# Performance work log

Measured on AMD Instinct MI355X. Metric: run time of the kernel, lower is better.

Reference implementation:

```python
import jax, jax.numpy as jnp
import numpy as np
from jax import lax

B = 32
ITERS = 100
ALPHA = 0.3  # keras LeakyReLU default alpha
BN_SCALE = np.float32(1.0 / np.sqrt(1.0 + 1e-3))  # inference BN, default moving stats (mean 0, var 1)


def _make_psf_mat():
    # Gaussian PSF mapping 5184 fine (72x72) code positions -> 81 coarse (9x9) pixels, mat shape (5184, 81)
    sigma = (150.0 / 100.0) * 9.0 / 64.0
    coarse = np.arange(9) + 0.5
    fine = (np.arange(72) + 0.5) * 9.0 / 72.0
    g = np.exp(-(fine[:, None] - coarse[None, :]) ** 2 / (2.0 * sigma ** 2))  # (72, 9)
    mat = np.einsum('ia,jb->ijab', g, g).reshape(5184, 81)
    mat = mat / np.linalg.norm(mat, ord=2)  # spectral-normalize so FISTA (mu=1) is stable
    return mat.astype(np.float32)


def leaky(x):
    return jnp.where(x >= 0, x, ALPHA * x)


def conv(x, k, strides=(1, 1)):
    return lax.conv_general_dilated(x, k, strides, 'SAME',
                                    dimension_numbers=('NHWC', 'HWIO', 'NHWC'))


def _forward(inp, mat, w1_k, w1_b, x1_k, x1_b, c51_k, c51_b, c15_k, c15_b,
             c55_k, c55_b, x2_k, x2_b, y17_k, y17_b, y71_k, y71_b, yc_k, yc_b,
             d1_k, d2_k, h1_w, h1_b, h2_w, h2_b, h3_w, h3_b):
    b = inp.shape[0]
    # w branch
    w = leaky(conv(inp, w1_k) + w1_b)  # (B,9,9,1)
    # z branch -> lambda parameter
    z = inp * BN_SCALE
    z = leaky(conv(z, d1_k, strides=(3, 3)) * BN_SCALE)  # (B,3,3,12), downsample: conv no-bias + BN + LeakyReLU
    z = leaky(conv(z, d2_k, strides=(3, 3)) * BN_SCALE)  # (B,1,1,24)
    z = z.reshape(b, -1)
    z = z @ h1_w + h1_b
    z = z @ h2_w + h2_b
    z = z @ h3_w + h3_b  # (B,1)
    param = 0.1 * jax.nn.sigmoid(z)  # (B,1)
    # x branch: normalize (max of |x| over axis 1 only, as in source)
    x = inp / (0.001 + jnp.max(jnp.abs(inp), axis=1, keepdims=True))
    x = leaky(conv(x, x1_k) + x1_b)  # (B,9,9,3)
    # --- CompressedSensing: 100-iter FISTA, vectorized over batch and 3 channels ---
    im = x.reshape(b, 81, 3).transpose(0, 2, 1)  # (B,3,81) row-major flatten per channel
    lam = (param * 0.1)[:, :, None]  # (B,1,1), mu = 1.0

    def step(carry, _):
        y_tmp, y_last, t = carry
        resid = im - jnp.einsum('bcn,nk->bck', y_tmp, mat)      # (B,3,81)  = im - mat^T y
        re = jnp.einsum('bck,nk->bcn', resid, mat)              # (B,3,5184) = mat (im - mat^T y)
        wv = y_tmp + re
        y_new = jax.nn.relu(wv - lam) - jax.nn.relu(-wv - lam)  # soft threshold
        t_n = (1.0 + jnp.sqrt(1.0 + 4.0 * t * t)) / 2.0
        y_next = y_new + (t - 1.0) / t_n * (y_new - y_last)
        return (y_next, y_new, t_n), None

    init = (jnp.zeros((b, 3, 5184), jnp.float32),
            jnp.zeros((b, 3, 5184), jnp.float32),
            jnp.float32(1.0))
    (_, y_new, _), _ = lax.scan(step, init, None, length=ITERS)
    cs_out = y_new.transpose(0, 2, 1).reshape(b, 72, 72, 3)  # stack channels last then reshape
    x = conv(cs_out, c51_k, strides=(2, 2)) + c51_b   # (B,36,36,16), no activation
    x = conv(x, c15_k, strides=(2, 2)) + c15_b        # (B,18,18,32)
    x = conv(x, c55_k, strides=(2, 2)) + c55_b        # (B,9,9,64)
    x = leaky(conv(x, x2_k) + x2_b)                   # (B,9,9,8)
    # y branch
    y1 = conv(inp, y17_k) + y17_b                     # (B,9,9,32)
    y2 = conv(inp, y71_k) + y71_b                     # (B,9,9,32)
    y = leaky(conv(jnp.concatenate([y1, y2], axis=-1), yc_k) + yc_b)  # (B,9,9,32)
    out = jnp.concatenate([w, x, y], axis=-1)         # (B,9,9,41)
    return out, cs_out


def setup_inputs() -> dict:
    key = jax.random.key(0)
    ks = jax.random.split(key, 20)
    rn = lambda k, s, sc=0.1: sc * jax.random.normal(k, s, dtype=jnp.float32)
    x1_k = jnp.clip(1.0 + 0.3 * jax.random.normal(ks[1], (1, 1, 3, 3)), 0.0, None).astype(jnp.float32)
    return {
        'inp': jax.random.normal(ks[0], (B, 9, 9, 3), dtype=jnp.float32),
        'mat': jnp.asarray(_make_psf_mat()),
        'w1_k': rn(ks[2], (1, 1, 3, 1)), 'w1_b': jnp.zeros((1,), jnp.float32),
        'x1_k': x1_k, 'x1_b': jnp.zeros((3,), jnp.float32),
        'c51_k': rn(ks[3], (5, 1, 3, 16)), 'c51_b': jnp.zeros((16,), jnp.float32),
        'c15_k': rn(ks[4], (1, 5, 16, 32)), 'c15_b': jnp.zeros((32,), jnp.float32),
        'c55_k': rn(ks[5], (5, 5, 32, 64)), 'c55_b': jnp.zeros((64,), jnp.float32),
        'x2_k': rn(ks[6], (1, 1, 64, 8)), 'x2_b': jnp.zeros((8,), jnp.float32),
        'y17_k': rn(ks[7], (1, 7, 3, 32)), 'y17_b': jnp.zeros((32,), jnp.float32),
        'y71_k': rn(ks[8], (7, 1, 3, 32)), 'y71_b': jnp.zeros((32,), jnp.float32),
        'yc_k': rn(ks[9], (1, 1, 64, 32)), 'yc_b': jnp.zeros((32,), jnp.float32),
        'd1_k': rn(ks[10], (5, 5, 3, 12)), 'd2_k': rn(ks[11], (5, 5, 12, 24)),
        'h1_w': rn(ks[12], (24, 24), 0.2), 'h1_b': jnp.zeros((24,), jnp.float32),
        'h2_w': rn(ks[13], (24, 12), 0.2), 'h2_b': jnp.zeros((12,), jnp.float32),
        'h3_w': rn(ks[14], (12, 1), 0.2), 'h3_b': jnp.zeros((1,), jnp.float32),
    }


def reference(inp, mat, w1_k, w1_b, x1_k, x1_b, c51_k, c51_b, c15_k, c15_b,
              c55_k, c55_b, x2_k, x2_b, y17_k, y17_b, y71_k, y71_b, yc_k, yc_b,
              d1_k, d2_k, h1_w, h1_b, h2_w, h2_b, h3_w, h3_b):
    return _forward(inp, mat, w1_k, w1_b, x1_k, x1_b, c51_k, c51_b, c15_k, c15_b,
                    c55_k, c55_b, x2_k, x2_b, y17_k, y17_b, y71_k, y71_b, yc_k, yc_b,
                    d1_k, d2_k, h1_w, h1_b, h2_w, h2_b, h3_w, h3_b)
```

## Files before the change

kernel.cpp:

```cpp
#include <hip/hip_runtime.h>
#include <math.h>

#define LEAKY(x) ((x) >= 0.f ? (x) : 0.3f*(x))

#define G_OFF   0
#define IM_OFF  648
#define LAM_OFF 8424
#define WB_OFF  8456
#define YBR_OFF 11048
#define X1_OFF  93992
#define X2_OFF  757544
#define X3_OFF  1089320

#define OUT0 106272

__global__ __launch_bounds__(256) void prep_kernel(
    const float* __restrict__ inp, const float* __restrict__ mat,
    const float* __restrict__ w1_k, const float* __restrict__ w1_b,
    const float* __restrict__ x1_k, const float* __restrict__ x1_b,
    const float* __restrict__ y17_k, const float* __restrict__ y17_b,
    const float* __restrict__ y71_k, const float* __restrict__ y71_b,
    const float* __restrict__ yc_k, const float* __restrict__ yc_b,
    const float* __restrict__ d1_k, const float* __restrict__ d2_k,
    const float* __restrict__ h1_w, const float* __restrict__ h1_b,
    const float* __restrict__ h2_w, const float* __restrict__ h2_b,
    const float* __restrict__ h3_w, const float* __restrict__ h3_b,
    float* __restrict__ ws)
{
    int t = threadIdx.x;
    if (blockIdx.x == 0) {
        float rs = rsqrtf(mat[0]);
        for (int u = t; u < 648; u += 256) {
            int i = u / 9, a = u % 9;
            ws[G_OFF + u] = mat[(size_t)(i*72)*81 + a*9] * rs;
        }
        return;
    }
    int b = blockIdx.x - 1;
    __shared__ float sin_[243];
    __shared__ float cm[27];
    __shared__ float cat[5184];
    __shared__ float z1[108];
    __shared__ float z2[24];
    __shared__ float v1[24];
    __shared__ float v2[12];

    const float BN  = 1.0f / sqrtf(1.001f);
    const float BN2 = BN * BN;

    for (int u = t; u < 243; u += 256) sin_[u] = inp[b*243 + u];
    __syncthreads();

    if (t < 81) {
        float s = w1_b[0];
        for (int i = 0; i < 3; ++i) s += sin_[t*3+i] * w1_k[i];
        ws[WB_OFF + b*81 + t] = LEAKY(s);
    } else if (t < 108) {
        int u = t - 81;
        float m = 0.f;
        for (int r = 0; r < 9; ++r) m = fmaxf(m, fabsf(sin_[r*27 + u]));
        cm[u] = 0.001f + m;
    }
    if (t >= 128 && t < 236) {
        int u = t - 128;
        int o = u % 12, ox = (u/12) % 3, oy = u/36;
        float s = 0.f;
        for (int kh = 0; kh < 5; ++kh) {
            int iy = oy*3 - 1 + kh;
            if (iy < 0 || iy > 8) continue;
            for (int kw = 0; kw < 5; ++kw) {
                int ix = ox*3 - 1 + kw;
                if (ix < 0 || ix > 8) continue;
                for (int i = 0; i < 3; ++i)
                    s += sin_[(iy*9+ix)*3 + i] * d1_k[((kh*5+kw)*3 + i)*12 + o];
            }
        }
        z1[u] = LEAKY(BN2 * s);
    }
    __syncthreads();

    if (t < 243) {
        int o = t / 81, p = t % 81;
        int c = p % 9;
        float s = x1_b[o];
        for (int i = 0; i < 3; ++i)
            s += (sin_[p*3+i] / cm[c*3+i]) * x1_k[i*3 + o];
        ws[IM_OFF + (b*3 + o)*81 + p] = LEAKY(s);
    }
    __syncthreads();

    if (t < 24) {
        float s = 0.f;
        for (int kh = 1; kh < 4; ++kh)
            for (int kw = 1; kw < 4; ++kw)
                for (int i = 0; i < 12; ++i)
                    s += z1[((kh-1)*3 + (kw-1))*12 + i] * d2_k[((kh*5+kw)*12 + i)*24 + t];
        z2[t] = LEAKY(BN * s);
    }
    __syncthreads();
    if (t < 24) {
        float s = h1_b[t];
        for (int i = 0; i < 24; ++i) s += z2[i] * h1_w[i*24 + t];
        v1[t] = s;
    }
    __syncthreads();
    if (t < 12) {
        float s = h2_b[t];
        for (int i = 0; i < 24; ++i) s += v1[i] * h2_w[i*12 + t];
        v2[t] = s;
    }
    __syncthreads();
    if (t == 0) {
        float s = h3_b[0];
        for (int i = 0; i < 12; ++i) s += v2[i] * h3_w[i];
        ws[LAM_OFF + b] = 0.01f / (1.f + expf(-s));
    }

    for (int u = t; u < 5184; u += 256) {
        int pos = u / 64, i = u % 64;
        int r = pos / 9, c = pos % 9;
        float s;
        if (i < 32) {
            s = y17_b[i];
            for (int kw = 0; kw < 7; ++kw) {
                int cc = c - 3 + kw;
                if (cc < 0 || cc > 8) continue;
                for (int ii = 0; ii < 3; ++ii)
                    s += sin_[(r*9+cc)*3 + ii] * y17_k[(kw*3+ii)*32 + i];
            }
        } else {
            int i2 = i - 32;
            s = y71_b[i2];
            for (int kh = 0; kh < 7; ++kh) {
                int rr = r - 3 + kh;
                if (rr < 0 || rr > 8) continue;
                for (int ii = 0; ii < 3; ++ii)
                    s += sin_[(rr*9+c)*3 + ii] * y71_k[(kh*3+ii)*32 + i2];
            }
        }
        cat[pos*64 + i] = s;
    }
    __syncthreads();
    for (int u = t; u < 2592; u += 256) {
        int pos = u / 32, o = u % 32;
        float s = yc_b[o];
        for (int i = 0; i < 64; ++i) s += cat[pos*64 + i] * yc_k[i*32 + o];
        ws[YBR_OFF + (b*81 + pos)*32 + o] = LEAKY(s);
    }
}

__global__ __launch_bounds__(512, 2) void fista_kernel(
    const float* __restrict__ ws, float* __restrict__ cs_out)
{
    __shared__ __align__(16) float Qt[648];
    __shared__ __align__(16) float U[9*432];
    __shared__ __align__(16) float T[9*76];
    __shared__ __align__(16) float P[6*84];
    __shared__ __align__(16) float R[108];

    int t = threadIdx.x;
    int b = blockIdx.x / 3, ch = blockIdx.x % 3;
    const float* g = ws + G_OFF;
    float lam = ws[LAM_OFF + b];

    int j = t % 72, grp = t / 72;
    bool act = t < 432;

    float Gr[108];
    if (act) {
#pragma unroll
        for (int s = 0; s < 12; ++s)
#pragma unroll
            for (int a = 0; a < 9; ++a)
                Gr[s*9 + a] = g[(grp*12 + s)*9 + a];
    }
    float Gj[9];
    if (act) {
#pragma unroll
        for (int a = 0; a < 9; ++a) Gj[a] = g[j*9 + a];
    }
    int pa = t / 54, prem = t % 54, pb = prem / 6, pseg = prem % 6;
    float GTr[12];
    if (t < 486) {
#pragma unroll
        for (int r = 0; r < 12; ++r) GTr[r] = g[(pseg*12 + r)*9 + pb];
    }
    float im_ab = 0.f;
    if (t < 81) im_ab = ws[IM_OFF + (b*3 + ch)*81 + t];
    if (t < 108) {
        int a = t / 12, c = t % 12;
        R[t] = (c < 9) ? ws[IM_OFF + (b*3 + ch)*81 + a*9 + c] : 0.f;
    }

    float Yv[12], Yl[12];
#pragma unroll
    for (int s = 0; s < 12; ++s) { Yv[s] = 0.f; Yl[s] = 0.f; }
    float tk = 1.f;
    __syncthreads();

    for (int it = 0; it < 100; ++it) {
        if (act) {
            const float4* R4 = (const float4*)(R + grp*12);
            float4 r0 = R4[0], r1 = R4[1], r2 = R4[2];
            Qt[grp*72 + j] =
                r0.x*Gj[0] + r0.y*Gj[1] + r0.z*Gj[2] + r0.w*Gj[3]
              + r1.x*Gj[4] + r1.y*Gj[5] + r1.z*Gj[6] + r1.w*Gj[7]
              + r2.x*Gj[8];
        }
        if (t < 216) {
            int a2 = 6 + t/72;
            const float4* R4 = (const float4*)(R + a2*12);
            float4 r0 = R4[0], r1 = R4[1], r2 = R4[2];
            Qt[a2*72 + j] =
                r0.x*Gj[0] + r0.y*Gj[1] + r0.z*Gj[2] + r0.w*Gj[3]
              + r1.x*Gj[4] + r1.y*Gj[5] + r1.z*Gj[6] + r1.w*Gj[7]
              + r2.x*Gj[8];
        }
        __syncthreads();
        float tn = 0.5f*(1.f + sqrtf(1.f + 4.f*tk*tk));
        float cmom = (tk - 1.f) / tn;
        tk = tn;
        if (act) {
            float q0 = Qt[0*72+j], q1 = Qt[1*72+j], q2 = Qt[2*72+j],
                  q3 = Qt[3*72+j], q4 = Qt[4*72+j], q5 = Qt[5*72+j],
                  q6 = Qt[6*72+j], q7 = Qt[7*72+j], q8 = Qt[8*72+j];
            float u0=0,u1=0,u2=0,u3=0,u4=0,u5=0,u6=0,u7=0,u8=0;
#pragma unroll
            for (int s = 0; s < 12; ++s) {
                float re = Gr[s*9+0]*q0 + Gr[s*9+1]*q1 + Gr[s*9+2]*q2
                         + Gr[s*9+3]*q3 + Gr[s*9+4]*q4 + Gr[s*9+5]*q5
                         + Gr[s*9+6]*q6 + Gr[s*9+7]*q7 + Gr[s*9+8]*q8;
                float wv = Yv[s] + re;
                float aa = fabsf(wv) - lam;
                float yn = aa > 0.f ? copysignf(aa, wv) : 0.f;
                float yx = yn + cmom*(yn - Yl[s]);
                Yl[s] = yn; Yv[s] = yx;
                u0 += yx*Gr[s*9+0]; u1 += yx*Gr[s*9+1]; u2 += yx*Gr[s*9+2];
                u3 += yx*Gr[s*9+3]; u4 += yx*Gr[s*9+4]; u5 += yx*Gr[s*9+5];
                u6 += yx*Gr[s*9+6]; u7 += yx*Gr[s*9+7]; u8 += yx*Gr[s*9+8];
            }
            U[0*432+t]=u0; U[1*432+t]=u1; U[2*432+t]=u2; U[3*432+t]=u3;
            U[4*432+t]=u4; U[5*432+t]=u5; U[6*432+t]=u6; U[7*432+t]=u7;
            U[8*432+t]=u8;
        }
        if (it == 99) break;
        __syncthreads();
        if (act) {
            float s = U[grp*432 + j]       + U[grp*432 + 72 + j]
                    + U[grp*432 + 144 + j] + U[grp*432 + 216 + j]
                    + U[grp*432 + 288 + j] + U[grp*432 + 360 + j];
            T[grp*76 + j] = s;
        }
        if (t < 216) {
            int a2 = 6 + t/72;
            float s = U[a2*432 + j]       + U[a2*432 + 72 + j]
                    + U[a2*432 + 144 + j] + U[a2*432 + 216 + j]
                    + U[a2*432 + 288 + j] + U[a2*432 + 360 + j];
            T[a2*76 + j] = s;
        }
        __syncthreads();
        if (t < 486) {
            const float4* T4 = (const float4*)(T + pa*76 + pseg*12);
            float4 t0 = T4[0], t1 = T4[1], t2 = T4[2];
            P[pseg*84 + pa*9 + pb] =
                t0.x*GTr[0] + t0.y*GTr[1] + t0.z*GTr[2] + t0.w*GTr[3]
              + t1.x*GTr[4] + t1.y*GTr[5] + t1.z*GTr[6] + t1.w*GTr[7]
              + t2.x*GTr[8] + t2.y*GTr[9] + t2.z*GTr[10]+ t2.w*GTr[11];
        }
        __syncthreads();
        if (t < 81) {
            float s = P[t] + P[84+t] + P[168+t] + P[252+t] + P[336+t] + P[420+t];
            R[(t/9)*12 + (t%9)] = im_ab - s;
        }
        __syncthreads();
    }
    if (act) {
#pragma unroll
        for (int s = 0; s < 12; ++s) {
            int i = grp*12 + s;
            cs_out[(size_t)(b*5184 + i*72 + j)*3 + ch] = Yl[s];
        }
    }
}

__global__ __launch_bounds__(256) void c51_kernel(
    const float* __restrict__ cs, const float* __restrict__ k,
    const float* __restrict__ bias, float* __restrict__ out)
{
    int id = blockIdx.x*256 + threadIdx.x;
    if (id >= 32*36*36*16) return;
    int o = id & 15; int rest = id >> 4;
    int ox = rest % 36; rest /= 36; int oy = rest % 36; int b = rest / 36;
    float s = bias[o];
    int ix = ox*2;
    for (int kh = 0; kh < 5; ++kh) {
        int iy = oy*2 - 1 + kh;
        if (iy < 0 || iy >= 72) continue;
        const float* p = cs + ((size_t)(b*72 + iy)*72 + ix)*3;
        const float* kk = k + kh*48 + o;
        s += p[0]*kk[0] + p[1]*kk[16] + p[2]*kk[32];
    }
    out[id] = s;
}

__global__ __launch_bounds__(256) void c15_kernel(
    const float* __restrict__ x1, const float* __restrict__ k,
    const float* __restrict__ bias, float* __restrict__ out)
{
    int id = blockIdx.x*256 + threadIdx.x;
    if (id >= 32*18*18*32) return;
    int o = id & 31; int rest = id >> 5;
    int ox = rest % 18; rest /= 18; int oy = rest % 18; int b = rest / 18;
    float s = bias[o];
    int iy = oy*2;
    for (int kw = 0; kw < 5; ++kw) {
        int ix = ox*2 - 1 + kw;
        if (ix < 0 || ix >= 36) continue;
        const float* p = x1 + ((size_t)(b*36 + iy)*36 + ix)*16;
        const float* kk = k + kw*512 + o;
        for (int i = 0; i < 16; ++i) s += p[i]*kk[i*32];
    }
    out[id] = s;
}

__global__ __launch_bounds__(256) void c55_kernel(
    const float* __restrict__ x2, const float* __restrict__ k,
    const float* __restrict__ bias, float* __restrict__ out)
{
    int id = blockIdx.x*256 + threadIdx.x;
    if (id >= 32*9*9*64) return;
    int o = id & 63; int rest = id >> 6;
    int ox = rest % 9; rest /= 9; int oy = rest % 9; int b = rest / 9;
    float s = bias[o];
    for (int kh = 0; kh < 5; ++kh) {
        int iy = oy*2 - 1 + kh;
        if (iy < 0 || iy >= 18) continue;
        for (int kw = 0; kw < 5; ++kw) {
            int ix = ox*2 - 1 + kw;
            if (ix < 0 || ix >= 18) continue;
            const float* p = x2 + ((size_t)(b*18 + iy)*18 + ix)*32;
            const float* kk = k + (kh*5+kw)*2048 + o;
            for (int i = 0; i < 32; ++i) s += p[i]*kk[i*64];
        }
    }
    out[id] = s;
}

__global__ __launch_bounds__(256) void out_kernel(
    const float* __restrict__ ws, const float* __restrict__ x2_k,
    const float* __restrict__ x2_b, float* __restrict__ out)
{
    int id = blockIdx.x*256 + threadIdx.x;
    if (id >= OUT0) return;
    int q = id % 41; int rest = id / 41;
    int cc = rest % 9; rest /= 9; int r = rest % 9; int b = rest / 9;
    float val;
    if (q == 0) {
        val = ws[WB_OFF + b*81 + r*9 + cc];
    } else if (q <= 8) {
        int o = q - 1;
        const float* p = ws + X3_OFF + ((size_t)(b*9 + r)*9 + cc)*64;
        float s = x2_b[o];
        for (int i = 0; i < 64; ++i) s += p[i]*x2_k[i*8 + o];
        val = LEAKY(s);
    } else {
        val = ws[YBR_OFF + ((size_t)(b*81 + r*9 + cc))*32 + (q - 9)];
    }
    out[id] = val;
}

extern "C" void kernel_launch(void* const* d_in, const int* in_sizes, int n_in,
                              void* d_out, int out_size, void* d_ws, size_t ws_size,
                              hipStream_t stream) {
    const float* inp   = (const float*)d_in[0];
    const float* mat   = (const float*)d_in[1];
    const float* w1_k  = (const float*)d_in[2];
    const float* w1_b  = (const float*)d_in[3];
    const float* x1_k  = (const float*)d_in[4];
    const float* x1_b  = (const float*)d_in[5];
    const float* c51_k = (const float*)d_in[6];
    const float* c51_b = (const float*)d_in[7];
    const float* c15_k = (const float*)d_in[8];
    const float* c15_b = (const float*)d_in[9];
    const float* c55_k = (const float*)d_in[10];
    const float* c55_b = (const float*)d_in[11];
    const float* x2_k  = (const float*)d_in[12];
    const float* x2_b  = (const float*)d_in[13];
    const float* y17_k = (const float*)d_in[14];
    const float* y17_b = (const float*)d_in[15];
    const float* y71_k = (const float*)d_in[16];
    const float* y71_b = (const float*)d_in[17];
    const float* yc_k  = (const float*)d_in[18];
    const float* yc_b  = (const float*)d_in[19];
    const float* d1_k  = (const float*)d_in[20];
    const float* d2_k  = (const float*)d_in[21];
    const float* h1_w  = (const float*)d_in[22];
    const float* h1_b  = (const float*)d_in[23];
    const float* h2_w  = (const float*)d_in[24];
    const float* h2_b  = (const float*)d_in[25];
    const float* h3_w  = (const float*)d_in[26];
    const float* h3_b  = (const float*)d_in[27];

    float* ws  = (float*)d_ws;
    float* out = (float*)d_out;
    float* cs  = out + OUT0;

    hipLaunchKernelGGL(prep_kernel, dim3(33), dim3(256), 0, stream,
        inp, mat, w1_k, w1_b, x1_k, x1_b, y17_k, y17_b, y71_k, y71_b,
        yc_k, yc_b, d1_k, d2_k, h1_w, h1_b, h2_w, h2_b, h3_w, h3_b, ws);
    hipLaunchKernelGGL(fista_kernel, dim3(96), dim3(512), 0, stream, ws, cs);
    hipLaunchKernelGGL(c51_kernel, dim3(2592), dim3(256), 0, stream, cs, c51_k, c51_b, ws + X1_OFF);
    hipLaunchKernelGGL(c15_kernel, dim3(1296), dim3(256), 0, stream, ws + X1_OFF, c15_k, c15_b, ws + X2_OFF);
    hipLaunchKernelGGL(c55_kernel, dim3(648), dim3(256), 0, stream, ws + X2_OFF, c55_k, c55_b, ws + X3_OFF);
    hipLaunchKernelGGL(out_kernel, dim3(416), dim3(256), 0, stream, ws, x2_k, x2_b, out);
}
```

Baseline: 403.0 us.

## Restructure FISTA iteration to cut block barriers from five to three

Each thread now recomputes the full 9-element Qt vector from R in registers instead of a shared Qt stage, removing one barrier. The separate reduction of U over row groups and the following GT product are merged into one stage that reads U and a transposed G from shared memory, removing another barrier. Soft-thresholding is rewritten as a clamp-and-subtract, and the final iteration skips the U stores. The cost is redundant Qt arithmetic and more shared-memory reads per thread, in exchange for fewer synchronisations in the latency-bound 100-iteration loop.

Measured after the change: 464.9 us. +15.4%, slower.

```diff
diff --git a/kernel.cpp b/kernel.cpp
--- a/kernel.cpp
+++ b/kernel.cpp
@@ -152,9 +152,8 @@
 __global__ __launch_bounds__(512, 2) void fista_kernel(
     const float* __restrict__ ws, float* __restrict__ cs_out)
 {
-    __shared__ __align__(16) float Qt[648];
-    __shared__ __align__(16) float U[9*432];
-    __shared__ __align__(16) float T[9*76];
+    __shared__ __align__(16) float U[9*436];
+    __shared__ __align__(16) float Gt[9*76];
     __shared__ __align__(16) float P[6*84];
     __shared__ __align__(16) float R[108];
 
@@ -179,17 +178,17 @@
 #pragma unroll
         for (int a = 0; a < 9; ++a) Gj[a] = g[j*9 + a];
     }
-    int pa = t / 54, prem = t % 54, pb = prem / 6, pseg = prem % 6;
-    float GTr[12];
-    if (t < 486) {
-#pragma unroll
-        for (int r = 0; r < 12; ++r) GTr[r] = g[(pseg*12 + r)*9 + pb];
-    }
+    int pa = t / 54, prem = t % 54, pb = prem / 6, pp = prem % 6;
+
+    for (int u = t; u < 648; u += 512) {
+        int jj = u / 9, bb = u % 9;
+        Gt[bb*76 + jj] = g[u];
+    }
+
     float im_ab = 0.f;
-    if (t < 81) im_ab = ws[IM_OFF + (b*3 + ch)*81 + t];
-    if (t < 108) {
-        int a = t / 12, c = t % 12;
-        R[t] = (c < 9) ? ws[IM_OFF + (b*3 + ch)*81 + a*9 + c] : 0.f;
+    if (t < 81) {
+        im_ab = ws[IM_OFF + (b*3 + ch)*81 + t];
+        R[(t/9)*12 + (t%9)] = im_ab;
     }
 
     float Yv[12], Yl[12];
@@ -199,81 +198,65 @@
     __syncthreads();
 
     for (int it = 0; it < 100; ++it) {
-        if (act) {
-            const float4* R4 = (const float4*)(R + grp*12);
-            float4 r0 = R4[0], r1 = R4[1], r2 = R4[2];
-            Qt[grp*72 + j] =
-                r0.x*Gj[0] + r0.y*Gj[1] + r0.z*Gj[2] + r0.w*Gj[3]
-              + r1.x*Gj[4] + r1.y*Gj[5] + r1.z*Gj[6] + r1.w*Gj[7]
-              + r2.x*Gj[8];
-        }
-        if (t < 216) {
-            int a2 = 6 + t/72;
-            const float4* R4 = (const float4*)(R + a2*12);
-            float4 r0 = R4[0], r1 = R4[1], r2 = R4[2];
-            Qt[a2*72 + j] =
-                r0.x*Gj[0] + r0.y*Gj[1] + r0.z*Gj[2] + r0.w*Gj[3]
-              + r1.x*Gj[4] + r1.y*Gj[5] + r1.z*Gj[6] + r1.w*Gj[7]
-              + r2.x*Gj[8];
-        }
-        __syncthreads();
         float tn = 0.5f*(1.f + sqrtf(1.f + 4.f*tk*tk));
         float cmom = (tk - 1.f) / tn;
         tk = tn;
+
         if (act) {
-            float q0 = Qt[0*72+j], q1 = Qt[1*72+j], q2 = Qt[2*72+j],
-                  q3 = Qt[3*72+j], q4 = Qt[4*72+j], q5 = Qt[5*72+j],
-                  q6 = Qt[6*72+j], q7 = Qt[7*72+j], q8 = Qt[8*72+j];
+            float qt[9];
+#pragma unroll
+            for (int a = 0; a < 9; ++a) {
+                const float4* R4 = (const float4*)(R + a*12);
+                float4 r0 = R4[0], r1 = R4[1];
+                float  r8 = R[a*12 + 8];
+                qt[a] = r0.x*Gj[0] + r0.y*Gj[1] + r0.z*Gj[2] + r0.w*Gj[3]
+                      + r1.x*Gj[4] + r1.y*Gj[5] + r1.z*Gj[6] + r1.w*Gj[7]
+                      + r8*Gj[8];
+            }
             float u0=0,u1=0,u2=0,u3=0,u4=0,u5=0,u6=0,u7=0,u8=0;
 #pragma unroll
             for (int s = 0; s < 12; ++s) {
-                float re = Gr[s*9+0]*q0 + Gr[s*9+1]*q1 + Gr[s*9+2]*q2
-                         + Gr[s*9+3]*q3 + Gr[s*9+4]*q4 + Gr[s*9+5]*q5
-                         + Gr[s*9+6]*q6 + Gr[s*9+7]*q7 + Gr[s*9+8]*q8;
+                float re = Gr[s*9+0]*qt[0] + Gr[s*9+1]*qt[1] + Gr[s*9+2]*qt[2]
+                         + Gr[s*9+3]*qt[3] + Gr[s*9+4]*qt[4] + Gr[s*9+5]*qt[5]
+                         + Gr[s*9+6]*qt[6] + Gr[s*9+7]*qt[7] + Gr[s*9+8]*qt[8];
                 float wv = Yv[s] + re;
-                float aa = fabsf(wv) - lam;
-                float yn = aa > 0.f ? copysignf(aa, wv) : 0.f;
+                float cl = fminf(fmaxf(wv, -lam), lam);
+                float yn = wv - cl;
                 float yx = yn + cmom*(yn - Yl[s]);
                 Yl[s] = yn; Yv[s] = yx;
                 u0 += yx*Gr[s*9+0]; u1 += yx*Gr[s*9+1]; u2 += yx*Gr[s*9+2];
                 u3 += yx*Gr[s*9+3]; u4 += yx*Gr[s*9+4]; u5 += yx*Gr[s*9+5];
                 u6 += yx*Gr[s*9+6]; u7 += yx*Gr[s*9+7]; u8 += yx*Gr[s*9+8];
             }
-            U[0*432+t]=u0; U[1*432+t]=u1; U[2*432+t]=u2; U[3*432+t]=u3;
-            U[4*432+t]=u4; U[5*432+t]=u5; U[6*432+t]=u6; U[7*432+t]=u7;
-            U[8*432+t]=u8;
+            if (it < 99) {
+                U[0*436+t]=u0; U[1*436+t]=u1; U[2*436+t]=u2; U[3*436+t]=u3;
+                U[4*436+t]=u4; U[5*436+t]=u5; U[6*436+t]=u6; U[7*436+t]=u7;
+                U[8*436+t]=u8;
+            }
         }
         if (it == 99) break;
         __syncthreads();
-        if (act) {
-            float s = U[grp*432 + j]       + U[grp*432 + 72 + j]
-                    + U[grp*432 + 144 + j] + U[grp*432 + 216 + j]
-                    + U[grp*432 + 288 + j] + U[grp*432 + 360 + j];
-            T[grp*76 + j] = s;
-        }
-        if (t < 216) {
-            int a2 = 6 + t/72;
-            float s = U[a2*432 + j]       + U[a2*432 + 72 + j]
-                    + U[a2*432 + 144 + j] + U[a2*432 + 216 + j]
-                    + U[a2*432 + 288 + j] + U[a2*432 + 360 + j];
-            T[a2*76 + j] = s;
+
+        if (t < 486) {
+            const float4* Ur = (const float4*)(U + pa*436 + pp*72);
+            const float4* Gt4 = (const float4*)(Gt + pb*76);
+            float s = 0.f;
+#pragma unroll
+            for (int c4 = 0; c4 < 18; ++c4) {
+                float4 uu = Ur[c4], gg = Gt4[c4];
+                s += uu.x*gg.x + uu.y*gg.y + uu.z*gg.z + uu.w*gg.w;
+            }
+            P[pp*84 + pa*9 + pb] = s;
         }
         __syncthreads();
-        if (t < 486) {
-            const float4* T4 = (const float4*)(T + pa*76 + pseg*12);
-            float4 t0 = T4[0], t1 = T4[1], t2 = T4[2];
-            P[pseg*84 + pa*9 + pb] =
-                t0.x*GTr[0] + t0.y*GTr[1] + t0.z*GTr[2] + t0.w*GTr[3]
-              + t1.x*GTr[4] + t1.y*GTr[5] + t1.z*GTr[6] + t1.w*GTr[7]
-              + t2.x*GTr[8] + t2.y*GTr[9] + t2.z*GTr[10]+ t2.w*GTr[11];
-        }
-        __syncthreads();
+
         if (t < 81) {
             float s = P[t] + P[84+t] + P[168+t] + P[252+t] + P[336+t] + P[420+t];
             R[(t/9)*12 + (t%9)] = im_ab - s;
         }
         __syncthreads();
     }
+
     if (act) {
 #pragma unroll
         for (int s = 0; s < 12; ++s) {
```
